# Kernel optimization log

Measured on AMD Instinct MI355X. Metric: run time of the kernel, lower is better.

## Reference

```python
import jax, jax.numpy as jnp
import numpy as np
from jax import lax

BOOST_STRENGTH = 0.5
WEIGHT_DENSITY = 0.05


def setup_inputs() -> dict:
    key = jax.random.key(0)
    k1, k2, k3, k4, k5 = jax.random.split(key, 5)
    batch, d_in, d_out = 16384, 512, 4096
    x = jax.random.normal(k1, (batch, d_in), dtype=jnp.float32)
    W = jax.random.normal(k2, (d_out, d_in), dtype=jnp.float32) * 0.05
    b = jax.random.normal(k3, (d_out,), dtype=jnp.float32) * 0.01
    w_mask = (jax.random.uniform(k4, (d_out, d_in)) < WEIGHT_DENSITY).astype(jnp.float32)
    # duty cycle buffer in [0, 0.1]
    duty_cycle = jax.random.uniform(k5, (d_out,), dtype=jnp.float32) * 0.1
    k = 205  # round(0.05 * 4096)
    return {"x": x, "W": W, "b": b, "w_mask": w_mask,
            "duty_cycle": duty_cycle, "k": k}


def reference(x, W, b, w_mask, duty_cycle, k):
    # SparseWeights: masked dense linear
    y = x @ (W * w_mask).T + b                      # [B, n]
    n = y.shape[-1]
    target_density = k / n
    # KWinners boosting: exp of duty-cycle deficit
    boost = jnp.exp(BOOST_STRENGTH * (target_density - duty_cycle))  # [n]
    boosted = y * boost                              # [B, n]
    # top-k threshold per row on boosted values
    thresh = lax.top_k(boosted, k)[0][..., -1:]      # [B, 1]
    # mask: keep ORIGINAL activations at winner positions
    return jnp.where(boosted >= thresh, y, 0.0)
```

## Files before the change

kernel.cpp:

```cpp
#include <hip/hip_runtime.h>
#include <stdint.h>
#include <math.h>


#define BATCH 16384
#define K_DIM 512
#define N_DIM 4096
#define RPB 4
#define MAXE 64
#define ROWS_A 64
#define XPAD 65

typedef float f32x4 __attribute__((ext_vector_type(4)));
typedef unsigned int u32;

__global__ void boost_kernel(const float* __restrict__ duty,
                             const int* __restrict__ kptr,
                             float* __restrict__ boost) {
  const int j = blockIdx.x * blockDim.x + threadIdx.x;
  if (j < N_DIM) {
    const float td = (float)((double)kptr[0] / (double)N_DIM);
    const float arg = 0.5f * (td - duty[j]);
    boost[j] = (float)exp((double)arg);
  }
}

__global__ __launch_bounds__(256) void compress_kernel(
    const float* __restrict__ W, const float* __restrict__ mask,
    unsigned short* __restrict__ cIdx, float* __restrict__ cVal,
    int* __restrict__ cnt) {
  const int j = blockIdx.x * 4 + (threadIdx.x >> 6);
  const int lane = threadIdx.x & 63;
  if (j >= N_DIM) return;
  const float* mr = mask + (size_t)j * K_DIM;
  const float* wr = W + (size_t)j * K_DIM;
  int base = 0;
#pragma unroll
  for (int c = 0; c < K_DIM / 64; ++c) {
    const int k = c * 64 + lane;
    const bool act = (mr[k] != 0.0f);
    const unsigned long long bal = __ballot(act);
    const int pos = __popcll(bal & ((1ull << lane) - 1ull));
    if (act && base + pos < MAXE) {
      cIdx[(size_t)j * MAXE + base + pos] = (unsigned short)k;
      cVal[(size_t)j * MAXE + base + pos] = wr[k];
    }
    base += (int)__popcll(bal);
  }
  if (lane == 0) cnt[j] = base < MAXE ? base : MAXE;
}

__global__ __launch_bounds__(256) void fillA_kernel(
    const unsigned short* __restrict__ cIdx, const float* __restrict__ cVal,
    const int* __restrict__ cnt, uint2* __restrict__ pairsA) {
  const int idx = blockIdx.x * 256 + threadIdx.x;
  const int j = idx >> 6;
  const int e = idx & 63;
  uint2 pr;
  if (e < cnt[j]) {
    pr.x = (u32)cIdx[(size_t)j * MAXE + e] * (u32)XPAD;
    pr.y = __float_as_uint(cVal[(size_t)j * MAXE + e]);
  } else {
    pr.x = 0u; pr.y = 0u;
  }
  pairsA[idx] = pr;
}

__global__ __launch_bounds__(1024, 1) void fold_kernel(
    const float* __restrict__ x, const uint2* __restrict__ pairsA,
    const int* __restrict__ cnt, float* __restrict__ y) {
  __shared__ float xT[K_DIM * XPAD];
  const int tid = threadIdx.x;
  const int lane = tid & 63;
  const int wave = __builtin_amdgcn_readfirstlane(tid >> 6);
  const int row0 = blockIdx.x * ROWS_A;

#pragma unroll 1
  for (int i = 0; i < (ROWS_A * K_DIM) / 1024; ++i) {
    const int flat = i * 1024 + tid;
    const int row = flat >> 9;
    const int k = flat & (K_DIM - 1);
    xT[k * XPAD + row] = x[(size_t)(row0 + row) * K_DIM + k];
  }
  __syncthreads();

  const int jbase = wave * (N_DIM / 16);

#pragma unroll 1
  for (int g = 0; g < 8; ++g) {
    float acc[32];
#pragma unroll
    for (int q = 0; q < 32; ++q) acc[q] = 0.0f;

#pragma unroll
    for (int c4 = 0; c4 < 8; ++c4) {
      const int j0 = jbase + g * 32 + c4 * 4;
      const int4 cn = *(const int4*)(cnt + j0);
      int cmax = cn.x > cn.y ? cn.x : cn.y;
      cmax = cn.z > cmax ? cn.z : cmax;
      cmax = cn.w > cmax ? cn.w : cmax;
      const uint2* p0 = pairsA + (size_t)(j0 + 0) * MAXE;
      const uint2* p1 = pairsA + (size_t)(j0 + 1) * MAXE;
      const uint2* p2 = pairsA + (size_t)(j0 + 2) * MAXE;
      const uint2* p3 = pairsA + (size_t)(j0 + 3) * MAXE;
      float a0 = 0.0f, a1 = 0.0f, a2 = 0.0f, a3 = 0.0f;
      int e = 0;
#pragma unroll 1
      for (; e + 4 <= cmax; e += 4) {
#pragma unroll
        for (int q = 0; q < 4; ++q) {
          const uint2 e0 = p0[e + q];
          const uint2 e1 = p1[e + q];
          const uint2 e2 = p2[e + q];
          const uint2 e3 = p3[e + q];
          a0 = fmaf(__uint_as_float(e0.y), xT[e0.x + lane], a0);
          a1 = fmaf(__uint_as_float(e1.y), xT[e1.x + lane], a1);
          a2 = fmaf(__uint_as_float(e2.y), xT[e2.x + lane], a2);
          a3 = fmaf(__uint_as_float(e3.y), xT[e3.x + lane], a3);
        }
      }
#pragma unroll 1
      for (; e < cmax; ++e) {
        const uint2 e0 = p0[e];
        const uint2 e1 = p1[e];
        const uint2 e2 = p2[e];
        const uint2 e3 = p3[e];
        a0 = fmaf(__uint_as_float(e0.y), xT[e0.x + lane], a0);
        a1 = fmaf(__uint_as_float(e1.y), xT[e1.x + lane], a1);
        a2 = fmaf(__uint_as_float(e2.y), xT[e2.x + lane], a2);
        a3 = fmaf(__uint_as_float(e3.y), xT[e3.x + lane], a3);
      }
      acc[c4 * 4 + 0] = a0;
      acc[c4 * 4 + 1] = a1;
      acc[c4 * 4 + 2] = a2;
      acc[c4 * 4 + 3] = a3;
    }

    float* yp = y + (size_t)(row0 + lane) * N_DIM + jbase + g * 32;
#pragma unroll
    for (int q = 0; q < 8; ++q)
      *(f32x4*)(yp + q * 4) =
          (f32x4){acc[q * 4], acc[q * 4 + 1], acc[q * 4 + 2], acc[q * 4 + 3]};
  }
}

__global__ __launch_bounds__(256) void select_kernel(
    const float* __restrict__ bvec, const float* __restrict__ boost,
    const int* __restrict__ kptr, float* __restrict__ out) {
  __shared__ u32 hist4[4 * 256];
  __shared__ u32 hist[256];
  __shared__ u32 s_prefix, s_kk;
  const int tid = threadIdx.x;
  const int wave = tid >> 6;
  const int row0 = blockIdx.x * RPB;
  const int kk0 = kptr[0];

#pragma unroll 1
  for (int r = 0; r < RPB; ++r) {
    __syncthreads();
    float* orow = out + (size_t)(row0 + r) * N_DIM;

    float yv[16];
    u32 key[16];
    const f32x4* yp = (const f32x4*)orow + tid * 4;
    const f32x4* bp = (const f32x4*)bvec + tid * 4;
    const f32x4* gp = (const f32x4*)boost + tid * 4;
#pragma unroll
    for (int v = 0; v < 4; ++v) {
      const f32x4 a = yp[v], b = bp[v], c = gp[v];
#pragma unroll
      for (int q = 0; q < 4; ++q) {
        const float yy = a[q] + b[q];
        const float t = yy * c[q];
        const u32 u = __float_as_uint(t);
        yv[v * 4 + q] = yy;
        key[v * 4 + q] = (u & 0x80000000u) ? ~u : (u | 0x80000000u);
      }
    }
    if (tid == 0) { s_prefix = 0u; s_kk = (u32)kk0; }

#pragma unroll 1
    for (int round = 0; round < 4; ++round) {
      const int shift = 24 - 8 * round;
      const u32 himask = round ? (0xFFFFFFFFu << (32 - 8 * round)) : 0u;
      hist4[tid] = 0u; hist4[tid + 256] = 0u;
      hist4[tid + 512] = 0u; hist4[tid + 768] = 0u;
      __syncthreads();
      const u32 prefix = s_prefix;
      const u32 kk = s_kk;
#pragma unroll
      for (int u2 = 0; u2 < 16; ++u2)
        if ((key[u2] & himask) == prefix)
          atomicAdd(&hist4[wave * 256 + ((key[u2] >> shift) & 255u)], 1u);
      __syncthreads();
      hist[tid] = hist4[tid] + hist4[tid + 256] +
                  hist4[tid + 512] + hist4[tid + 768];
      __syncthreads();
      if (tid < 64) {
        const int l = tid;
        const u32 h0 = hist[l * 4], h1 = hist[l * 4 + 1];
        const u32 h2 = hist[l * 4 + 2], h3 = hist[l * 4 + 3];
        const u32 s3 = h3, s2 = h2 + s3, s1 = h1 + s2, s0 = h0 + s1;
        u32 t = s0;
#pragma unroll
        for (int off = 1; off < 64; off <<= 1) {
          const u32 v = __shfl_down(t, off, 64);
          if (l + off < 64) t += v;
        }
        const u32 Eab = t - s0;
        const u32 S[5] = {Eab + s0, Eab + s1, Eab + s2, Eab + s3, Eab};
#pragma unroll
        for (int i = 0; i < 4; ++i)
          if (S[i] >= kk && S[i + 1] < kk) {
            s_prefix = prefix | ((u32)(l * 4 + i) << shift);
            s_kk = kk - S[i + 1];
          }
      }
      __syncthreads();
    }
    const u32 tkey = s_prefix;

    f32x4* op = (f32x4*)orow + tid * 4;
#pragma unroll
    for (int v = 0; v < 4; ++v) {
      f32x4 o;
#pragma unroll
      for (int q = 0; q < 4; ++q)
        o[q] = (key[v * 4 + q] >= tkey) ? yv[v * 4 + q] : 0.0f;
      op[v] = o;
    }
  }
}

extern "C" void kernel_launch(void* const* d_in, const int* in_sizes, int n_in,
                              void* d_out, int out_size, void* d_ws, size_t ws_size,
                              hipStream_t stream) {
  const float* x     = (const float*)d_in[0];
  const float* W     = (const float*)d_in[1];
  const float* bvec  = (const float*)d_in[2];
  const float* wmask = (const float*)d_in[3];
  const float* duty  = (const float*)d_in[4];
  const int* kptr    = (const int*)d_in[5];
  float* out = (float*)d_out;

  uint8_t* ws = (uint8_t*)d_ws;
  unsigned short* cIdx = (unsigned short*)(ws);
  float* cVal          = (float*)(ws + (1u << 20));
  int* cnt             = (int*)(ws + (2u << 20));
  float* boost         = (float*)(ws + (2u << 20) + (64u << 10));
  uint2* pairsA        = (uint2*)(ws + (4u << 20));

  boost_kernel<<<16, 256, 0, stream>>>(duty, kptr, boost);
  compress_kernel<<<N_DIM / 4, 256, 0, stream>>>(W, wmask, cIdx, cVal, cnt);
  fillA_kernel<<<(N_DIM * MAXE) / 256, 256, 0, stream>>>(cIdx, cVal, cnt, pairsA);
  fold_kernel<<<BATCH / ROWS_A, 1024, 0, stream>>>(x, pairsA, cnt, out);
  select_kernel<<<BATCH / RPB, 256, 0, stream>>>(bvec, boost, kptr, out);
}
```

Before: 743.3 us.

## Prefetch padded weight pairs with wide loads and use wave-level bitwise top-k select

The fold kernel now pads each output's (index, weight) pair list to 72 entries and reads it with 128-bit vector loads. It double-buffers these loads one 8-entry chunk ahead so the fetches overlap the LDS gathers and FMAs. A VGPR zero offset keeps the loads on the vector path. The select kernel drops the block-wide 4-round radix histogram with LDS atomics and barriers; instead one wave handles each row and finds the threshold with a 32-step bitwise search using ballot and popcount, which uses many more instructions but needs no shared memory or synchronisation.

Measured after the change: 1.133 ms. 1.52x slower.

```diff
diff --git a/kernel.cpp b/kernel.cpp
--- a/kernel.cpp
+++ b/kernel.cpp
@@ -6,13 +6,15 @@
 #define BATCH 16384
 #define K_DIM 512
 #define N_DIM 4096
-#define RPB 4
 #define MAXE 64
+#define PSTRIDE 72
 #define ROWS_A 64
 #define XPAD 65
 
 typedef float f32x4 __attribute__((ext_vector_type(4)));
 typedef unsigned int u32;
+typedef unsigned long long u64;
+typedef u64 u64x2 __attribute__((ext_vector_type(2)));
 
 __global__ void boost_kernel(const float* __restrict__ duty,
                              const int* __restrict__ kptr,
@@ -54,8 +56,8 @@
     const unsigned short* __restrict__ cIdx, const float* __restrict__ cVal,
     const int* __restrict__ cnt, uint2* __restrict__ pairsA) {
   const int idx = blockIdx.x * 256 + threadIdx.x;
-  const int j = idx >> 6;
-  const int e = idx & 63;
+  const int j = idx / PSTRIDE;
+  const int e = idx - j * PSTRIDE;
   uint2 pr;
   if (e < cnt[j]) {
     pr.x = (u32)cIdx[(size_t)j * MAXE + e] * (u32)XPAD;
@@ -63,7 +65,7 @@
   } else {
     pr.x = 0u; pr.y = 0u;
   }
-  pairsA[idx] = pr;
+  pairsA[(size_t)j * PSTRIDE + e] = pr;
 }
 
 __global__ __launch_bounds__(1024, 1) void fold_kernel(
@@ -75,6 +77,9 @@
   const int wave = __builtin_amdgcn_readfirstlane(tid >> 6);
   const int row0 = blockIdx.x * ROWS_A;
 
+  u32 vz;
+  asm volatile("v_mov_b32 %0, 0" : "=v"(vz));
+
 #pragma unroll 1
   for (int i = 0; i < (ROWS_A * K_DIM) / 1024; ++i) {
     const int flat = i * 1024 + tid;
@@ -99,36 +104,48 @@
       int cmax = cn.x > cn.y ? cn.x : cn.y;
       cmax = cn.z > cmax ? cn.z : cmax;
       cmax = cn.w > cmax ? cn.w : cmax;
-      const uint2* p0 = pairsA + (size_t)(j0 + 0) * MAXE;
-      const uint2* p1 = pairsA + (size_t)(j0 + 1) * MAXE;
-      const uint2* p2 = pairsA + (size_t)(j0 + 2) * MAXE;
-      const uint2* p3 = pairsA + (size_t)(j0 + 3) * MAXE;
+      const int cm8 = (cmax + 7) & ~7;
+      const u64* q0 = (const u64*)(pairsA + (size_t)(j0 + 0) * PSTRIDE) + vz;
+      const u64* q1 = (const u64*)(pairsA + (size_t)(j0 + 1) * PSTRIDE) + vz;
+      const u64* q2 = (const u64*)(pairsA + (size_t)(j0 + 2) * PSTRIDE) + vz;
+      const u64* q3 = (const u64*)(pairsA + (size_t)(j0 + 3) * PSTRIDE) + vz;
       float a0 = 0.0f, a1 = 0.0f, a2 = 0.0f, a3 = 0.0f;
-      int e = 0;
-#pragma unroll 1
-      for (; e + 4 <= cmax; e += 4) {
-#pragma unroll
-        for (int q = 0; q < 4; ++q) {
-          const uint2 e0 = p0[e + q];
-          const uint2 e1 = p1[e + q];
-          const uint2 e2 = p2[e + q];
-          const uint2 e3 = p3[e + q];
-          a0 = fmaf(__uint_as_float(e0.y), xT[e0.x + lane], a0);
-          a1 = fmaf(__uint_as_float(e1.y), xT[e1.x + lane], a1);
-          a2 = fmaf(__uint_as_float(e2.y), xT[e2.x + lane], a2);
-          a3 = fmaf(__uint_as_float(e3.y), xT[e3.x + lane], a3);
-        }
-      }
-#pragma unroll 1
-      for (; e < cmax; ++e) {
-        const uint2 e0 = p0[e];
-        const uint2 e1 = p1[e];
-        const uint2 e2 = p2[e];
-        const uint2 e3 = p3[e];
-        a0 = fmaf(__uint_as_float(e0.y), xT[e0.x + lane], a0);
-        a1 = fmaf(__uint_as_float(e1.y), xT[e1.x + lane], a1);
-        a2 = fmaf(__uint_as_float(e2.y), xT[e2.x + lane], a2);
-        a3 = fmaf(__uint_as_float(e3.y), xT[e3.x + lane], a3);
+      u64x2 A0[2], A1[2], A2[2], A3[2];
+      A0[0] = *(const u64x2*)(q0);     A0[1] = *(const u64x2*)(q0 + 2);
+      A1[0] = *(const u64x2*)(q1);     A1[1] = *(const u64x2*)(q1 + 2);
+      A2[0] = *(const u64x2*)(q2);     A2[1] = *(const u64x2*)(q2 + 2);
+      A3[0] = *(const u64x2*)(q3);     A3[1] = *(const u64x2*)(q3 + 2);
+#pragma unroll 1
+      for (int e = 0; e < cm8; e += 8) {
+        u64x2 B0[2], B1[2], B2[2], B3[2];
+        B0[0] = *(const u64x2*)(q0 + e + 4); B0[1] = *(const u64x2*)(q0 + e + 6);
+        B1[0] = *(const u64x2*)(q1 + e + 4); B1[1] = *(const u64x2*)(q1 + e + 6);
+        B2[0] = *(const u64x2*)(q2 + e + 4); B2[1] = *(const u64x2*)(q2 + e + 6);
+        B3[0] = *(const u64x2*)(q3 + e + 4); B3[1] = *(const u64x2*)(q3 + e + 6);
+#pragma unroll
+        for (int h = 0; h < 2; ++h)
+#pragma unroll
+          for (int q = 0; q < 2; ++q) {
+            const u64 e0 = A0[h][q], e1 = A1[h][q], e2 = A2[h][q], e3 = A3[h][q];
+            a0 = fmaf(__uint_as_float((u32)(e0 >> 32)), xT[(u32)e0 + lane], a0);
+            a1 = fmaf(__uint_as_float((u32)(e1 >> 32)), xT[(u32)e1 + lane], a1);
+            a2 = fmaf(__uint_as_float((u32)(e2 >> 32)), xT[(u32)e2 + lane], a2);
+            a3 = fmaf(__uint_as_float((u32)(e3 >> 32)), xT[(u32)e3 + lane], a3);
+          }
+        A0[0] = *(const u64x2*)(q0 + e + 8); A0[1] = *(const u64x2*)(q0 + e + 10);
+        A1[0] = *(const u64x2*)(q1 + e + 8); A1[1] = *(const u64x2*)(q1 + e + 10);
+        A2[0] = *(const u64x2*)(q2 + e + 8); A2[1] = *(const u64x2*)(q2 + e + 10);
+        A3[0] = *(const u64x2*)(q3 + e + 8); A3[1] = *(const u64x2*)(q3 + e + 10);
+#pragma unroll
+        for (int h = 0; h < 2; ++h)
+#pragma unroll
+          for (int q = 0; q < 2; ++q) {
+            const u64 e0 = B0[h][q], e1 = B1[h][q], e2 = B2[h][q], e3 = B3[h][q];
+            a0 = fmaf(__uint_as_float((u32)(e0 >> 32)), xT[(u32)e0 + lane], a0);
+            a1 = fmaf(__uint_as_float((u32)(e1 >> 32)), xT[(u32)e1 + lane], a1);
+            a2 = fmaf(__uint_as_float((u32)(e2 >> 32)), xT[(u32)e2 + lane], a2);
+            a3 = fmaf(__uint_as_float((u32)(e3 >> 32)), xT[(u32)e3 + lane], a3);
+          }
       }
       acc[c4 * 4 + 0] = a0;
       acc[c4 * 4 + 1] = a1;
@@ -147,88 +164,48 @@
 __global__ __launch_bounds__(256) void select_kernel(
     const float* __restrict__ bvec, const float* __restrict__ boost,
     const int* __restrict__ kptr, float* __restrict__ out) {
-  __shared__ u32 hist4[4 * 256];
-  __shared__ u32 hist[256];
-  __shared__ u32 s_prefix, s_kk;
-  const int tid = threadIdx.x;
-  const int wave = tid >> 6;
-  const int row0 = blockIdx.x * RPB;
-  const int kk0 = kptr[0];
-
-#pragma unroll 1
-  for (int r = 0; r < RPB; ++r) {
-    __syncthreads();
-    float* orow = out + (size_t)(row0 + r) * N_DIM;
-
-    float yv[16];
-    u32 key[16];
-    const f32x4* yp = (const f32x4*)orow + tid * 4;
-    const f32x4* bp = (const f32x4*)bvec + tid * 4;
-    const f32x4* gp = (const f32x4*)boost + tid * 4;
-#pragma unroll
-    for (int v = 0; v < 4; ++v) {
-      const f32x4 a = yp[v], b = bp[v], c = gp[v];
-#pragma unroll
-      for (int q = 0; q < 4; ++q) {
-        const float yy = a[q] + b[q];
-        const float t = yy * c[q];
-        const u32 u = __float_as_uint(t);
-        yv[v * 4 + q] = yy;
-        key[v * 4 + q] = (u & 0x80000000u) ? ~u : (u | 0x80000000u);
-      }
+  const int lane = threadIdx.x & 63;
+  const int row = blockIdx.x * 4 + (threadIdx.x >> 6);
+  const u32 kk = (u32)kptr[0];
+  float* orow = out + (size_t)row * N_DIM;
+
+  float yv[64];
+  u32 kv[64];
+#pragma unroll
+  for (int v = 0; v < 16; ++v) {
+    const int j = v * 256 + lane * 4;
+    const f32x4 a = *(const f32x4*)(orow + j);
+    const f32x4 b = *(const f32x4*)(bvec + j);
+    const f32x4 c = *(const f32x4*)(boost + j);
+#pragma unroll
+    for (int q = 0; q < 4; ++q) {
+      const float yy = a[q] + b[q];
+      const float t = yy * c[q];
+      const u32 u = __float_as_uint(t);
+      yv[v * 4 + q] = yy;
+      kv[v * 4 + q] = (u & 0x80000000u) ? ~u : (u | 0x80000000u);
     }
-    if (tid == 0) { s_prefix = 0u; s_kk = (u32)kk0; }
-
-#pragma unroll 1
-    for (int round = 0; round < 4; ++round) {
-      const int shift = 24 - 8 * round;
-      const u32 himask = round ? (0xFFFFFFFFu << (32 - 8 * round)) : 0u;
-      hist4[tid] = 0u; hist4[tid + 256] = 0u;
-      hist4[tid + 512] = 0u; hist4[tid + 768] = 0u;
-      __syncthreads();
-      const u32 prefix = s_prefix;
-      const u32 kk = s_kk;
-#pragma unroll
-      for (int u2 = 0; u2 < 16; ++u2)
-        if ((key[u2] & himask) == prefix)
-          atomicAdd(&hist4[wave * 256 + ((key[u2] >> shift) & 255u)], 1u);
-      __syncthreads();
-      hist[tid] = hist4[tid] + hist4[tid + 256] +
-                  hist4[tid + 512] + hist4[tid + 768];
-      __syncthreads();
-      if (tid < 64) {
-        const int l = tid;
-        const u32 h0 = hist[l * 4], h1 = hist[l * 4 + 1];
-        const u32 h2 = hist[l * 4 + 2], h3 = hist[l * 4 + 3];
-        const u32 s3 = h3, s2 = h2 + s3, s1 = h1 + s2, s0 = h0 + s1;
-        u32 t = s0;
-#pragma unroll
-        for (int off = 1; off < 64; off <<= 1) {
-          const u32 v = __shfl_down(t, off, 64);
-          if (l + off < 64) t += v;
-        }
-        const u32 Eab = t - s0;
-        const u32 S[5] = {Eab + s0, Eab + s1, Eab + s2, Eab + s3, Eab};
-#pragma unroll
-        for (int i = 0; i < 4; ++i)
-          if (S[i] >= kk && S[i + 1] < kk) {
-            s_prefix = prefix | ((u32)(l * 4 + i) << shift);
-            s_kk = kk - S[i + 1];
-          }
-      }
-      __syncthreads();
-    }
-    const u32 tkey = s_prefix;
-
-    f32x4* op = (f32x4*)orow + tid * 4;
-#pragma unroll
-    for (int v = 0; v < 4; ++v) {
-      f32x4 o;
-#pragma unroll
-      for (int q = 0; q < 4; ++q)
-        o[q] = (key[v * 4 + q] >= tkey) ? yv[v * 4 + q] : 0.0f;
-      op[v] = o;
-    }
+  }
+
+  u32 P = 0u;
+#pragma unroll 1
+  for (int bit = 31; bit >= 0; --bit) {
+    const u32 C = P | (1u << bit);
+    u32 c = 0u;
+#pragma unroll
+    for (int s = 0; s < 64; ++s)
+      c += (u32)__popcll(__ballot(kv[s] >= C));
+    if (c >= kk) P = C;
+  }
+
+#pragma unroll
+  for (int v = 0; v < 16; ++v) {
+    const int j = v * 256 + lane * 4;
+    f32x4 o;
+#pragma unroll
+    for (int q = 0; q < 4; ++q)
+      o[q] = (kv[v * 4 + q] >= P) ? yv[v * 4 + q] : 0.0f;
+    *(f32x4*)(orow + j) = o;
   }
 }
 
@@ -248,11 +225,12 @@
   float* cVal          = (float*)(ws + (1u << 20));
   int* cnt             = (int*)(ws + (2u << 20));
   float* boost         = (float*)(ws + (2u << 20) + (64u << 10));
-  uint2* pairsA        = (uint2*)(ws + (4u << 20));
+  uint2* pairsA        = (uint2*)(ws + (3u << 20));
 
   boost_kernel<<<16, 256, 0, stream>>>(duty, kptr, boost);
   compress_kernel<<<N_DIM / 4, 256, 0, stream>>>(W, wmask, cIdx, cVal, cnt);
-  fillA_kernel<<<(N_DIM * MAXE) / 256, 256, 0, stream>>>(cIdx, cVal, cnt, pairsA);
+  fillA_kernel<<<(N_DIM * PSTRIDE) / 256, 256, 0, stream>>>(cIdx, cVal, cnt,
+                                                            pairsA);
   fold_kernel<<<BATCH / ROWS_A, 1024, 0, stream>>>(x, pairsA, cnt, out);
-  select_kernel<<<BATCH / RPB, 256, 0, stream>>>(bvec, boost, kptr, out);
-}
+  select_kernel<<<BATCH / 4, 256, 0, stream>>>(bvec, boost, kptr, out);
+}
```
